# Kernel tuning notes

Hardware: AMD Instinct MI355X
Metric: run time of the kernel (lower is better)

## Reference

```python
import jax, jax.numpy as jnp
import numpy as np


def _conv1x1(x, W, b):
    # x: (n, c_in, h, w); W: (c_out, c_in); b: (c_out,)
    return jnp.einsum('nchw,oc->nohw', x, W) + b[None, :, None, None]


def setup_inputs() -> dict:
    key = jax.random.key(0)
    ks = jax.random.split(key, 9)
    n, C, h, w = 2, 256, 64, 64
    Ch = C // 2
    s_in = 0.02
    return {
        'feature': jax.random.normal(ks[0], (n, C, h, w), dtype=jnp.float32),
        'Wq': jax.random.normal(ks[1], (Ch, C), dtype=jnp.float32) * s_in,
        'bq': jax.random.normal(ks[2], (Ch,), dtype=jnp.float32) * s_in,
        'Wk': jax.random.normal(ks[3], (Ch, C), dtype=jnp.float32) * s_in,
        'bk': jax.random.normal(ks[4], (Ch,), dtype=jnp.float32) * s_in,
        'Wv': jax.random.normal(ks[5], (Ch, C), dtype=jnp.float32) * s_in,
        'bv': jax.random.normal(ks[6], (Ch,), dtype=jnp.float32) * s_in,
        'Wm': jax.random.normal(ks[7], (C, Ch), dtype=jnp.float32) * s_in,
        'bm': jax.random.normal(ks[8], (C,), dtype=jnp.float32) * s_in,
    }


def reference(feature, Wq, bq, Wk, bk, Wv, bv, Wm, bm):
    n, C, h, w = feature.shape
    Ch = C // 2
    N = n * h * w
    # 1x1 conv projections, then flatten batch+spatial into one sequence dim
    q = _conv1x1(feature, Wq, bq)  # (n, Ch, h, w)
    k = _conv1x1(feature, Wk, bk)
    v = _conv1x1(feature, Wv, bv)
    # NCHW -> NHWC -> (N, Ch), matching torch transpose(1,2).transpose(2,3).reshape
    q = jnp.transpose(q, (0, 2, 3, 1)).reshape(N, Ch)
    k = jnp.transpose(k, (0, 2, 3, 1)).reshape(N, Ch)
    v = jnp.transpose(v, (0, 2, 3, 1)).reshape(N, Ch)
    # scores = k @ q.T (note: torch code uses k as rows, q.T as cols)
    scores = k @ q.T  # (N, N)
    attn = jax.nn.softmax(scores, axis=-1)
    mask = attn @ v  # (N, Ch)
    mask = mask.reshape(n, h, w, Ch)
    # torch transpose chain (2,3)->(1,2)->(2,3): (n,h,w,Ch) -> (n,Ch,w,h)
    mask = jnp.transpose(mask, (0, 3, 2, 1))
    out = _conv1x1(mask, Wm, bm)  # (n, C, w, h); h==w so residual add is valid
    return out + feature
```

## Files before the change

### kernel.cpp

```cpp
#include <hip/hip_runtime.h>
#include <hip/hip_bf16.h>

#define LOG2E 1.44269504088896340736f

typedef __attribute__((ext_vector_type(8))) short short8;
typedef __attribute__((ext_vector_type(4))) float f32x4;
typedef __attribute__((ext_vector_type(2))) unsigned int uint2v;
typedef __attribute__((ext_vector_type(4))) unsigned int uint4v;
typedef unsigned int u32;

__device__ __forceinline__ short f2bf(float f) {
    unsigned u = __builtin_bit_cast(unsigned, f);
    unsigned r = (u + 0x7FFFu + ((u >> 16) & 1u)) >> 16;
    return (short)r;
}

__device__ __forceinline__ float bf2f(short x) {
    unsigned u = ((unsigned)(unsigned short)x) << 16;
    return __builtin_bit_cast(float, u);
}

__device__ __forceinline__ unsigned cvt_pk_bf16(float lo, float hi) {
    unsigned r;
    asm volatile("v_cvt_pk_bf16_f32 %0, %1, %2" : "=v"(r) : "v"(lo), "v"(hi));
    return r;
}

__device__ __forceinline__ float fexp2(float x) {
    float r;
    asm("v_exp_f32 %0, %1" : "=v"(r) : "v"(x));
    return r;
}

#define WAIT_BAR4 { asm volatile("s_waitcnt vmcnt(4)" ::: "memory"); \
                    __builtin_amdgcn_s_barrier(); \
                    __builtin_amdgcn_sched_barrier(0); }
#define WAIT_BAR0 { asm volatile("s_waitcnt vmcnt(0)" ::: "memory"); \
                    __builtin_amdgcn_s_barrier(); \
                    __builtin_amdgcn_sched_barrier(0); }

__global__ __launch_bounds__(64) void wprep_kernel(
    const float* __restrict__ Wq, const float* __restrict__ bq,
    const float* __restrict__ Wk, const float* __restrict__ bk,
    const float* __restrict__ Wv, const float* __restrict__ bv,
    const float* __restrict__ Wm,
    short* __restrict__ Wb, float* __restrict__ bqkv, short* __restrict__ Wmb)
{
    const int b = blockIdx.x;
    const int t = threadIdx.x;
    if (b < 384) {
        const int mat = b >> 7, row = b & 127;
        const float* src = (mat == 0 ? Wq : mat == 1 ? Wk : Wv) + (size_t)row * 256;
        const float sc = (mat == 1) ? LOG2E : 1.f;
        float4 v = *(const float4*)(src + t * 4);
        uint2v pk;
        pk.x = cvt_pk_bf16(v.x * sc, v.y * sc);
        pk.y = cvt_pk_bf16(v.z * sc, v.w * sc);
        *(uint2v*)(Wb + (size_t)b * 256 + t * 4) = pk;
    } else if (b == 384) {
        for (int e = t; e < 384; e += 64) {
            const int mat = e >> 7;
            const float* bsrc = (mat == 0 ? bq : mat == 1 ? bk : bv);
            bqkv[e] = bsrc[e & 127] * (mat == 1 ? LOG2E : 1.f);
        }
    } else {
        const int row = b - 385;
        float2 v = *(const float2*)(Wm + (size_t)row * 128 + t * 2);
        *(u32*)(Wmb + (size_t)row * 128 + t * 2) = cvt_pk_bf16(v.x, v.y);
    }
}

__global__ __launch_bounds__(256) void proj_kernel(
    const float* __restrict__ feat, const short* __restrict__ Wb,
    const float* __restrict__ bqkv,
    short* __restrict__ Qb, short* __restrict__ Kb, short* __restrict__ VTp)
{
    __shared__ __align__(16) short Xs[16 * 256];
    __shared__ __align__(16) short VTs[128 * 16];
    const int t = threadIdx.x;
    const int blk = blockIdx.x;
    const int ib = blk * 16;
    const int n = ib >> 12;
    const int hw0 = ib & 4095;

    {
        const int r = t & 15, cg = t >> 4;
        const float* fp = feat + (size_t)n * 1048576 + (size_t)(cg * 16) * 4096 + hw0 + r;
        short8 t0, t1;
        #pragma unroll
        for (int ci = 0; ci < 8; ++ci) {
            t0[ci] = f2bf(fp[(size_t)ci * 4096]);
            t1[ci] = f2bf(fp[(size_t)(ci + 8) * 4096]);
        }
        const int sw = (r & 7) << 2;
        *(short8*)(&Xs[r * 256 + ((cg * 2) ^ sw) * 8]) = t0;
        *(short8*)(&Xs[r * 256 + ((cg * 2 + 1) ^ sw) * 8]) = t1;
    }
    __syncthreads();

    const int lane = t & 63;
    const int w = __builtin_amdgcn_readfirstlane(t >> 6);
    const int l15 = lane & 15;
    const int g = lane >> 4;
    const int o0w = w * 96;

    f32x4 acc[6];
    #pragma unroll
    for (int osub = 0; osub < 6; ++osub)
        acc[osub] = *(const f32x4*)(bqkv + o0w + osub * 16 + 4 * g);

    const short* wbase = Wb + (size_t)(o0w + l15) * 256 + g * 8;
    const int xsw = (l15 & 7) << 2;
    #pragma unroll
    for (int kc = 0; kc < 8; ++kc) {
        short8 xf = *(const short8*)(&Xs[l15 * 256 + (((kc * 4 + g) ^ xsw) * 8)]);
        #pragma unroll
        for (int osub = 0; osub < 6; ++osub) {
            short8 wf = *(const short8*)(wbase + (size_t)osub * 16 * 256 + kc * 32);
            acc[osub] = __builtin_amdgcn_mfma_f32_16x16x32_bf16(wf, xf, acc[osub], 0, 0, 0);
        }
    }

    #pragma unroll
    for (int osub = 0; osub < 6; ++osub) {
        const int o0 = o0w + osub * 16;
        const int mat = o0 >> 7;
        const int col = (o0 & 127) + 4 * g;
        if (mat == 0) {
            uint2v pk;
            pk.x = cvt_pk_bf16(acc[osub][0], acc[osub][1]);
            pk.y = cvt_pk_bf16(acc[osub][2], acc[osub][3]);
            *(uint2v*)(Qb + (size_t)(ib + l15) * 128 + col) = pk;
        } else if (mat == 1) {
            uint2v pk;
            pk.x = cvt_pk_bf16(acc[osub][0], acc[osub][1]);
            pk.y = cvt_pk_bf16(acc[osub][2], acc[osub][3]);
            *(uint2v*)(Kb + (size_t)(ib + l15) * 128 + col) = pk;
        } else {
            #pragma unroll
            for (int reg = 0; reg < 4; ++reg)
                VTs[(col + reg) * 16 + l15] = f2bf(acc[osub][reg]);
        }
    }
    __syncthreads();

    {
        const int o = t >> 1, ih = (t & 1) * 8;
        short8 vv = *(const short8*)(&VTs[o * 16 + ih]);
        const int base32 = ib & ~31;
        const int u = (ib >> 4) & 1;
        const int p0 = 2 * ih + 4 * u;
        uint4v q = __builtin_bit_cast(uint4v, vv);
        uint2v lo; lo.x = q.x; lo.y = q.y;
        uint2v hi; hi.x = q.z; hi.y = q.w;
        *(uint2v*)(VTp + (size_t)o * 8192 + base32 + p0) = lo;
        *(uint2v*)(VTp + (size_t)o * 8192 + base32 + p0 + 8) = hi;
    }
}

__global__ __launch_bounds__(256, 2) void attn_kernel(
    const short* __restrict__ Qb, const short* __restrict__ Kb,
    const short* __restrict__ VTp,
    short* __restrict__ Opart, float* __restrict__ Ssb)
{
    __shared__ __align__(16) char smem[65536];

    const int tid = threadIdx.x;
    const int lane = tid & 63;
    const int w = __builtin_amdgcn_readfirstlane(tid >> 6);
    const int l15 = lane & 15;
    const int g = lane >> 4;
    const int blk = blockIdx.x;
    const int ibX = blk >> 4;
    const int jq  = blk & 15;
    const int iw  = ibX * 128 + w * 32;
    const int j0  = jq * 512;

    short8 kf[2][4];
    #pragma unroll
    for (int iset = 0; iset < 2; ++iset)
        #pragma unroll
        for (int dcq = 0; dcq < 4; ++dcq)
            kf[iset][dcq] = *(const short8*)(Kb + (size_t)(iw + iset * 16 + l15) * 128 + dcq * 32 + g * 8);

    f32x4 O[2][8];
    #pragma unroll
    for (int iset = 0; iset < 2; ++iset)
        #pragma unroll
        for (int dc = 0; dc < 8; ++dc) O[iset][dc] = (f32x4){0.f, 0.f, 0.f, 0.f};
    float s[2] = {0.f, 0.f};
    short8 pf[2];

    const short* srcQ0;
    const short* srcQ1;
    const short* srcV0;
    const short* srcV1;
    {
        int r0 = 4 * w + (lane >> 4), c0 = lane & 15;
        srcQ0 = Qb + (size_t)(j0 + r0) * 128 + (c0 ^ (r0 & 7)) * 8;
        int r1 = 16 + 4 * w + (lane >> 4);
        srcQ1 = Qb + (size_t)(j0 + r1) * 128 + (c0 ^ (r1 & 7)) * 8;
        int d0 = 16 * w + (lane >> 2), c2 = lane & 3;
        srcV0 = VTp + (size_t)d0 * 8192 + j0 + (c2 ^ (d0 & 3)) * 8;
        int d1 = 64 + 16 * w + (lane >> 2);
        srcV1 = VTp + (size_t)d1 * 8192 + j0 + (c2 ^ (d1 & 3)) * 8;
    }

    auto stage = [&](int quarter) {
        char* base = smem + quarter * 16384;
        __builtin_amdgcn_global_load_lds(
            (const __attribute__((address_space(1))) u32*)(const void*)srcQ0,
            (__attribute__((address_space(3))) u32*)(void*)(base + w * 1024), 16, 0, 0);
        __builtin_amdgcn_global_load_lds(
            (const __attribute__((address_space(1))) u32*)(const void*)srcQ1,
            (__attribute__((address_space(3))) u32*)(void*)(base + (4 + w) * 1024), 16, 0, 0);
        __builtin_amdgcn_global_load_lds(
            (const __attribute__((address_space(1))) u32*)(const void*)srcV0,
            (__attribute__((address_space(3))) u32*)(void*)(base + (8 + w) * 1024), 16, 0, 0);
        __builtin_amdgcn_global_load_lds(
            (const __attribute__((address_space(1))) u32*)(const void*)srcV1,
            (__attribute__((address_space(3))) u32*)(void*)(base + (12 + w) * 1024), 16, 0, 0);
        srcQ0 += 32 * 128;
        srcQ1 += 32 * 128;
        srcV0 += 32;
        srcV1 += 32;
    };

    auto QKSM = [&](const char* base) {
        const char* Qt = base;
        const int xs = (l15 & 7) << 4;

        f32x4 sv[2][2];
        #pragma unroll
        for (int jh = 0; jh < 2; ++jh)
            #pragma unroll
            for (int iset = 0; iset < 2; ++iset)
                sv[jh][iset] = (f32x4){-16.f, -16.f, -16.f, -16.f};

        #pragma unroll
        for (int dcq = 0; dcq < 4; ++dcq) {
            short8 qa0 = *(const short8*)(Qt + ((l15 * 256 + dcq * 64 + g * 16) ^ xs));
            short8 qa1 = *(const short8*)(Qt + (((l15 + 16) * 256 + dcq * 64 + g * 16) ^ xs));
            sv[0][0] = __builtin_amdgcn_mfma_f32_16x16x32_bf16(qa0, kf[0][dcq], sv[0][0], 0, 0, 0);
            sv[0][1] = __builtin_amdgcn_mfma_f32_16x16x32_bf16(qa0, kf[1][dcq], sv[0][1], 0, 0, 0);
            sv[1][0] = __builtin_amdgcn_mfma_f32_16x16x32_bf16(qa1, kf[0][dcq], sv[1][0], 0, 0, 0);
            sv[1][1] = __builtin_amdgcn_mfma_f32_16x16x32_bf16(qa1, kf[1][dcq], sv[1][1], 0, 0, 0);
        }

        #pragma unroll
        for (int iset = 0; iset < 2; ++iset) {
            float p0[4], p1[4], ps = 0.f;
            #pragma unroll
            for (int e = 0; e < 4; ++e) {
                p0[e] = fexp2(sv[0][iset][e]);
                p1[e] = fexp2(sv[1][iset][e]);
                ps += p0[e] + p1[e];
            }
            s[iset] += ps;
            uint4v pk;
            pk.x = cvt_pk_bf16(p0[0], p0[1]);
            pk.y = cvt_pk_bf16(p0[2], p0[3]);
            pk.z = cvt_pk_bf16(p1[0], p1[1]);
            pk.w = cvt_pk_bf16(p1[2], p1[3]);
            pf[iset] = __builtin_bit_cast(short8, pk);
        }
    };

    auto PV = [&](const char* base) {
        const char* Vt = base + 8192;
        const int xs = (l15 & 7) << 4;
        __builtin_amdgcn_s_setprio(1);
        #pragma unroll
        for (int dc = 0; dc < 8; ++dc) {
            short8 va = *(const short8*)(Vt + (dc * 16 + l15) * 64 + ((g ^ (l15 & 3)) << 4));
            O[0][dc] = __builtin_amdgcn_mfma_f32_16x16x32_bf16(va, pf[0], O[0][dc], 0, 0, 0);
            O[1][dc] = __builtin_amdgcn_mfma_f32_16x16x32_bf16(va, pf[1], O[1][dc], 0, 0, 0);
        }
        __builtin_amdgcn_s_setprio(0);
    };

    stage(0);
    stage(1);
    WAIT_BAR4;
    stage(2);
    QKSM(smem);
    for (int tt = 1; tt <= 13; ++tt) {
        WAIT_BAR4;
        stage(tt + 2);
        PV(smem + ((tt - 1) & 3) * 16384);
        QKSM(smem + (tt & 3) * 16384);
    }
    WAIT_BAR4;
    PV(smem + (13 & 3) * 16384);
    QKSM(smem + (14 & 3) * 16384);
    WAIT_BAR0;
    PV(smem + (14 & 3) * 16384);
    QKSM(smem + (15 & 3) * 16384);
    PV(smem + (15 & 3) * 16384);

    #pragma unroll
    for (int iset = 0; iset < 2; ++iset) {
        const int i = iw + iset * 16 + l15;
        #pragma unroll
        for (int dc = 0; dc < 8; ++dc) {
            uint2v pk;
            pk.x = cvt_pk_bf16(O[iset][dc][0], O[iset][dc][1]);
            pk.y = cvt_pk_bf16(O[iset][dc][2], O[iset][dc][3]);
            *(uint2v*)(Opart + (size_t)(jq * 8192 + i) * 128 + dc * 16 + 4 * g) = pk;
        }
        Ssb[(((size_t)jq * 8192 + i) << 2) + g] = s[iset];
    }
}

__global__ __launch_bounds__(256, 4) void epi_kernel(
    const short* __restrict__ Opart, const float* __restrict__ Ssb,
    const short* __restrict__ Wmb, const float* __restrict__ bm,
    const float* __restrict__ feat, float* __restrict__ out)
{
    __shared__ __align__(16) short Ms[16 * 128];
    const int t = threadIdx.x;
    const int blk = blockIdx.x;
    const int yt = blk & 3;
    const int x = (blk >> 2) & 63;
    const int n = blk >> 8;
    const int y0 = yt * 16;

    {
        const int r = t >> 4, c = t & 15;
        const int i = n * 4096 + (y0 + r) * 64 + x;
        float acc8[8] = {0.f, 0.f, 0.f, 0.f, 0.f, 0.f, 0.f, 0.f};
        #pragma unroll
        for (int q = 0; q < 16; ++q) {
            short8 o = *(const short8*)(Opart + ((size_t)q * 8192 + i) * 128 + c * 8);
            #pragma unroll
            for (int e = 0; e < 8; ++e) acc8[e] += bf2f(o[e]);
        }
        f32x4 s4 = *(const f32x4*)(Ssb + (((size_t)c * 8192 + i) << 2));
        float tp = (s4[0] + s4[1]) + (s4[2] + s4[3]);
        tp += __shfl_xor(tp, 1);
        tp += __shfl_xor(tp, 2);
        tp += __shfl_xor(tp, 4);
        tp += __shfl_xor(tp, 8);
        const float inv = 1.f / tp;
        uint4v pk;
        pk.x = cvt_pk_bf16(acc8[0] * inv, acc8[1] * inv);
        pk.y = cvt_pk_bf16(acc8[2] * inv, acc8[3] * inv);
        pk.z = cvt_pk_bf16(acc8[4] * inv, acc8[5] * inv);
        pk.w = cvt_pk_bf16(acc8[6] * inv, acc8[7] * inv);
        *(short8*)(&Ms[r * 128 + ((c ^ ((r & 7) << 1)) * 8)]) =
            __builtin_bit_cast(short8, pk);
    }
    __syncthreads();

    const int lane = t & 63;
    const int w = __builtin_amdgcn_readfirstlane(t >> 6);
    const int l15 = lane & 15;
    const int g = lane >> 4;
    const int c0 = w * 64;

    short8 bf[4];
    const int msw = (l15 & 7) << 1;
    #pragma unroll
    for (int dcq = 0; dcq < 4; ++dcq)
        bf[dcq] = *(const short8*)(&Ms[l15 * 128 + (((dcq * 4 + g) ^ msw) * 8)]);

    f32x4 acc[4];
    #pragma unroll
    for (int ct = 0; ct < 4; ++ct)
        acc[ct] = *(const f32x4*)(bm + c0 + ct * 16 + 4 * g);

    const short* wbase = Wmb + (size_t)(c0 + l15) * 128 + g * 8;
    #pragma unroll
    for (int dcq = 0; dcq < 4; ++dcq) {
        #pragma unroll
        for (int ct = 0; ct < 4; ++ct) {
            short8 wf = *(const short8*)(wbase + (size_t)ct * 16 * 128 + dcq * 32);
            acc[ct] = __builtin_amdgcn_mfma_f32_16x16x32_bf16(wf, bf[dcq], acc[ct], 0, 0, 0);
        }
    }

    #pragma unroll
    for (int ct = 0; ct < 4; ++ct) {
        #pragma unroll
        for (int reg = 0; reg < 4; ++reg) {
            const int c = c0 + ct * 16 + 4 * g + reg;
            const size_t oidx = (((size_t)(n * 256 + c) * 64 + x) * 64) + y0 + l15;
            out[oidx] = acc[ct][reg] + feat[oidx];
        }
    }
}

extern "C" void kernel_launch(void* const* d_in, const int* in_sizes, int n_in,
                              void* d_out, int out_size, void* d_ws, size_t ws_size,
                              hipStream_t stream) {
    const float* feat = (const float*)d_in[0];
    const float* Wq = (const float*)d_in[1];
    const float* bq = (const float*)d_in[2];
    const float* Wk = (const float*)d_in[3];
    const float* bk = (const float*)d_in[4];
    const float* Wv = (const float*)d_in[5];
    const float* bv = (const float*)d_in[6];
    const float* Wm = (const float*)d_in[7];
    const float* bm = (const float*)d_in[8];
    float* out = (float*)d_out;

    short* Qb = (short*)d_ws;
    short* Kb = Qb + 8192 * 128;
    short* VTp = Kb + 8192 * 128;
    short* Opart = VTp + 8192 * 128;
    float* Ssb = (float*)(Opart + (size_t)16 * 8192 * 128);
    float* bqkv = Ssb + (size_t)16 * 8192 * 4;
    short* Wb = (short*)(bqkv + 384);
    short* Wmb = Wb + 384 * 256;

    hipLaunchKernelGGL(wprep_kernel, dim3(641), dim3(64), 0, stream,
                       Wq, bq, Wk, bk, Wv, bv, Wm, Wb, bqkv, Wmb);
    hipLaunchKernelGGL(proj_kernel, dim3(512), dim3(256), 0, stream,
                       feat, Wb, bqkv, Qb, Kb, VTp);
    hipLaunchKernelGGL(attn_kernel, dim3(1024), dim3(256), 0, stream,
                       Qb, Kb, VTp, Opart, Ssb);
    hipLaunchKernelGGL(epi_kernel, dim3(512), dim3(256), 0, stream,
                       Opart, Ssb, Wmb, bm, feat, out);
}
```

Measured before the change: 79.72 us.

## Replace software-pipelined QK/PV schedule with double-staged loop and new V swizzle

```diff
diff --git a/kernel.cpp b/kernel.cpp
--- a/kernel.cpp
+++ b/kernel.cpp
@@ -31,13 +31,6 @@
     asm("v_exp_f32 %0, %1" : "=v"(r) : "v"(x));
     return r;
 }
-
-#define WAIT_BAR4 { asm volatile("s_waitcnt vmcnt(4)" ::: "memory"); \
-                    __builtin_amdgcn_s_barrier(); \
-                    __builtin_amdgcn_sched_barrier(0); }
-#define WAIT_BAR0 { asm volatile("s_waitcnt vmcnt(0)" ::: "memory"); \
-                    __builtin_amdgcn_s_barrier(); \
-                    __builtin_amdgcn_sched_barrier(0); }
 
 __global__ __launch_bounds__(64) void wprep_kernel(
     const float* __restrict__ Wq, const float* __restrict__ bq,
@@ -189,7 +182,6 @@
         #pragma unroll
         for (int dc = 0; dc < 8; ++dc) O[iset][dc] = (f32x4){0.f, 0.f, 0.f, 0.f};
     float s[2] = {0.f, 0.f};
-    short8 pf[2];
 
     const short* srcQ0;
     const short* srcQ1;
@@ -201,9 +193,9 @@
         int r1 = 16 + 4 * w + (lane >> 4);
         srcQ1 = Qb + (size_t)(j0 + r1) * 128 + (c0 ^ (r1 & 7)) * 8;
         int d0 = 16 * w + (lane >> 2), c2 = lane & 3;
-        srcV0 = VTp + (size_t)d0 * 8192 + j0 + (c2 ^ (d0 & 3)) * 8;
+        srcV0 = VTp + (size_t)d0 * 8192 + j0 + (c2 ^ ((d0 >> 1) & 3)) * 8;
         int d1 = 64 + 16 * w + (lane >> 2);
-        srcV1 = VTp + (size_t)d1 * 8192 + j0 + (c2 ^ (d1 & 3)) * 8;
+        srcV1 = VTp + (size_t)d1 * 8192 + j0 + (c2 ^ ((d1 >> 1) & 3)) * 8;
     }
 
     auto stage = [&](int quarter) {
@@ -226,8 +218,9 @@
         srcV1 += 32;
     };
 
-    auto QKSM = [&](const char* base) {
+    auto compute32 = [&](const char* base) {
         const char* Qt = base;
+        const char* Vt = base + 8192;
         const int xs = (l15 & 7) << 4;
 
         f32x4 sv[2][2];
@@ -237,6 +230,7 @@
             for (int iset = 0; iset < 2; ++iset)
                 sv[jh][iset] = (f32x4){-16.f, -16.f, -16.f, -16.f};
 
+        __builtin_amdgcn_s_setprio(1);
         #pragma unroll
         for (int dcq = 0; dcq < 4; ++dcq) {
             short8 qa0 = *(const short8*)(Qt + ((l15 * 256 + dcq * 64 + g * 16) ^ xs));
@@ -246,7 +240,9 @@
             sv[1][0] = __builtin_amdgcn_mfma_f32_16x16x32_bf16(qa1, kf[0][dcq], sv[1][0], 0, 0, 0);
             sv[1][1] = __builtin_amdgcn_mfma_f32_16x16x32_bf16(qa1, kf[1][dcq], sv[1][1], 0, 0, 0);
         }
-
+        __builtin_amdgcn_s_setprio(0);
+
+        short8 pf[2];
         #pragma unroll
         for (int iset = 0; iset < 2; ++iset) {
             float p0[4], p1[4], ps = 0.f;
@@ -264,15 +260,11 @@
             pk.w = cvt_pk_bf16(p1[2], p1[3]);
             pf[iset] = __builtin_bit_cast(short8, pk);
         }
-    };
-
-    auto PV = [&](const char* base) {
-        const char* Vt = base + 8192;
-        const int xs = (l15 & 7) << 4;
+
         __builtin_amdgcn_s_setprio(1);
         #pragma unroll
         for (int dc = 0; dc < 8; ++dc) {
-            short8 va = *(const short8*)(Vt + (dc * 16 + l15) * 64 + ((g ^ (l15 & 3)) << 4));
+            short8 va = *(const short8*)(Vt + (dc * 16 + l15) * 64 + ((g ^ ((l15 >> 1) & 3)) << 4));
             O[0][dc] = __builtin_amdgcn_mfma_f32_16x16x32_bf16(va, pf[0], O[0][dc], 0, 0, 0);
             O[1][dc] = __builtin_amdgcn_mfma_f32_16x16x32_bf16(va, pf[1], O[1][dc], 0, 0, 0);
         }
@@ -281,22 +273,16 @@
 
     stage(0);
     stage(1);
-    WAIT_BAR4;
-    stage(2);
-    QKSM(smem);
-    for (int tt = 1; tt <= 13; ++tt) {
-        WAIT_BAR4;
-        stage(tt + 2);
-        PV(smem + ((tt - 1) & 3) * 16384);
-        QKSM(smem + (tt & 3) * 16384);
-    }
-    WAIT_BAR4;
-    PV(smem + (13 & 3) * 16384);
-    QKSM(smem + (14 & 3) * 16384);
-    WAIT_BAR0;
-    PV(smem + (14 & 3) * 16384);
-    QKSM(smem + (15 & 3) * 16384);
-    PV(smem + (15 & 3) * 16384);
+    __syncthreads();
+    for (int tt = 0; tt < 16; tt += 2) {
+        if (tt + 2 < 16) {
+            stage((tt + 2) & 3);
+            stage((tt + 3) & 3);
+        }
+        compute32(smem + (tt & 3) * 16384);
+        compute32(smem + ((tt + 1) & 3) * 16384);
+        __syncthreads();
+    }
 
     #pragma unroll
     for (int iset = 0; iset < 2; ++iset) {
```

Result: no change. 78.52 us (-1.5%).
